# Kernel tuning notes

Measured on AMD Instinct MI355X. Metric: run time of the kernel, lower is better.

Reference implementation:

```python
import jax, jax.numpy as jnp
import numpy as np

B, H, W, C = 64, 56, 56, 128
WS, SHIFT, NH = 7, 3, 4
HD = C // NH            # 32
N = WS * WS             # 49 tokens per window
NW = (H // WS) * (W // WS)  # 64 windows per image
HID = 4 * C             # MLP hidden
EPS = 1e-5


def _rel_index():
    coords = np.stack(np.meshgrid(np.arange(WS), np.arange(WS), indexing='ij'))  # 2,ws,ws
    cf = coords.reshape(2, -1)                      # 2,N
    rel = (cf[:, :, None] - cf[:, None, :]).transpose(1, 2, 0)  # N,N,2
    rel[:, :, 0] += WS - 1
    rel[:, :, 1] += WS - 1
    rel[:, :, 0] *= 2 * WS - 1
    return rel.sum(-1).astype(np.int32)             # N,N in [0,(2ws-1)^2)


def _attn_mask():
    img = np.zeros((H, W))
    cnt = 0
    sl = (slice(0, -WS), slice(-WS, -SHIFT), slice(-SHIFT, None))
    for hs in sl:
        for ws_ in sl:
            img[hs, ws_] = cnt
            cnt += 1
    m = img.reshape(H // WS, WS, W // WS, WS).transpose(0, 2, 1, 3).reshape(-1, N)  # NW,N
    diff = m[:, None, :] - m[:, :, None]
    return np.where(diff != 0, -100.0, 0.0).astype(np.float32)  # NW,N,N


def setup_inputs() -> dict:
    key = jax.random.key(0)
    ks = jax.random.split(key, 14)
    s = 0.02
    inp = {
        'x': jax.random.normal(ks[0], (B, H * W, C), jnp.float32),
        'x_norm1': jax.random.normal(ks[1], (B, H * W, C), jnp.float32),
        'qkv_w': jax.random.normal(ks[2], (3 * C, C), jnp.float32) * s,
        'qkv_b': jnp.zeros((3 * C,), jnp.float32),
        'rel_bias_table': jax.random.normal(ks[3], ((2 * WS - 1) ** 2, NH), jnp.float32) * s,
        'proj_w': jax.random.normal(ks[4], (C, C), jnp.float32) * s,
        'proj_b': jnp.zeros((C,), jnp.float32),
        'norm2_w': jnp.ones((C,), jnp.float32),
        'norm2_b': jnp.zeros((C,), jnp.float32),
        'fc1_w': jax.random.normal(ks[5], (HID, C), jnp.float32) * s,
        'fc1_b': jnp.zeros((HID,), jnp.float32),
        'fc2_w': jax.random.normal(ks[6], (C, HID), jnp.float32) * s,
        'fc2_b': jnp.zeros((C,), jnp.float32),
        'attn_mask': jnp.asarray(_attn_mask()),
        'rel_index': jnp.asarray(_rel_index()),
    }
    return inp


def _ln(x, w, b):
    mu = x.mean(-1, keepdims=True)
    var = jnp.mean((x - mu) ** 2, axis=-1, keepdims=True)
    return (x - mu) * jax.lax.rsqrt(var + EPS) * w + b


def reference(x, x_norm1, qkv_w, qkv_b, rel_bias_table, proj_w, proj_b,
              norm2_w, norm2_b, fc1_w, fc1_b, fc2_w, fc2_b, attn_mask, rel_index):
    shortcut = x
    # cyclic shift + window partition
    xw = x_norm1.reshape(B, H, W, C)
    xw = jnp.roll(xw, (-SHIFT, -SHIFT), axis=(1, 2))
    win = xw.reshape(B, H // WS, WS, W // WS, WS, C).transpose(0, 1, 3, 2, 4, 5)
    win = win.reshape(B * NW, N, C)
    # windowed multi-head attention
    qkv = (win @ qkv_w.T + qkv_b).reshape(B * NW, N, 3, NH, HD).transpose(2, 0, 3, 1, 4)
    q, k, v = qkv[0], qkv[1], qkv[2]               # (B*NW, NH, N, HD)
    attn = jnp.einsum('whnd,whmd->whnm', q * (HD ** -0.5), k)
    bias = rel_bias_table[rel_index.reshape(-1)].reshape(N, N, NH).transpose(2, 0, 1)
    attn = attn + bias[None]
    attn = attn.reshape(B, NW, NH, N, N) + attn_mask[None, :, None]
    attn = jax.nn.softmax(attn.reshape(B * NW, NH, N, N), axis=-1)
    out = jnp.einsum('whnm,whmd->whnd', attn, v).transpose(0, 2, 1, 3).reshape(B * NW, N, C)
    out = out @ proj_w.T + proj_b
    # window reverse + reverse shift
    xw = out.reshape(B, H // WS, W // WS, WS, WS, C).transpose(0, 1, 3, 2, 4, 5).reshape(B, H, W, C)
    xw = jnp.roll(xw, (SHIFT, SHIFT), axis=(1, 2))
    x = shortcut + xw.reshape(B, H * W, C)
    # MLP (exact GELU, as torch default)
    h = _ln(x, norm2_w, norm2_b)
    h = jax.nn.gelu(h @ fc1_w.T + fc1_b, approximate=False)
    x = x + (h @ fc2_w.T + fc2_b)
    return x
```

## Files before the change

kernel.cpp:

```cpp
#include <hip/hip_runtime.h>
#include <hip/hip_bf16.h>
#include <math.h>

typedef __hip_bfloat16 bf16;
typedef __attribute__((ext_vector_type(8))) short short8;
typedef __attribute__((ext_vector_type(4))) short s4v;
typedef __attribute__((ext_vector_type(4))) float f32x4;

#define Bb 64
#define Hh 56
#define Ww 56
#define Cc 128
#define WS 7
#define SHIFT 3
#define NH 4
#define HD 32
#define Nn 49
#define NW 64
#define HID 512

#define WS_QKV 0
#define WS_PROJ 49152
#define WS_FC1 65536
#define WS_FC2 131072
#define WS_BIAS_BYTES 393216

__device__ __forceinline__ short fb(float v) { return __builtin_bit_cast(short, __float2bfloat16(v)); }

__device__ __forceinline__ float frcp(float d) {
    float r;
    asm("v_rcp_f32 %0, %1" : "=v"(r) : "v"(d));
    return r;
}

__device__ __forceinline__ float fgelu(float x) {
    float z = x * x;
    float u = fmaf(z, 0.0713537069f, 1.5957691216f);
    float e = __expf(u * x);
    float r = frcp(e + 1.f);
    return fmaf(-x, r, x);
}

__global__ __launch_bounds__(256) void prep_kernel(
    const float* __restrict__ qkv_w, const float* __restrict__ proj_w,
    const float* __restrict__ fc1_w, const float* __restrict__ fc2_w,
    const float* __restrict__ rel_bias, const int* __restrict__ rel_index,
    short* __restrict__ wsb, float* __restrict__ biasT)
{
    int t = blockIdx.x * 256 + threadIdx.x;
    if (t < 49152)       wsb[t] = fb(qkv_w[t]);
    else if (t < 65536)  wsb[t] = fb(proj_w[t - 49152]);
    else if (t < 131072) wsb[t] = fb(fc1_w[t - 65536]);
    else if (t < 196608) wsb[t] = fb(fc2_w[t - 131072]);
    if (t < 4 * Nn * Nn) {
        int h = t / (Nn * Nn), r = t - h * (Nn * Nn);
        biasT[t] = rel_bias[rel_index[r] * NH + h];
    }
}

#define SW 136
#define SQ 40
#define SV 72
#define SP 72

__global__ __launch_bounds__(512, 4) void attn_kernel(
    const float* __restrict__ x,
    const float* __restrict__ x_norm1,
    const float* __restrict__ qkv_b,
    const float* __restrict__ proj_b,
    const float* __restrict__ attn_mask,
    const short* __restrict__ wsb,
    const float* __restrict__ biasT,
    float* __restrict__ out)
{
    __shared__ short win[64 * SW];
    __shared__ short qk[2 * NH * 64 * SQ];
    __shared__ short vT[NH * HD * SV];

    const int blk = blockIdx.x;
    const int b   = blk >> 6;
    const int nw  = blk & 63;
    const int wh  = nw >> 3;
    const int wwi = nw & 7;
    const int tid  = threadIdx.x;
    const int wave = tid >> 6;
    const int lane = tid & 63;
    const int quad = lane >> 4;
    const int l16  = lane & 15;
    const int half = wave >> 2;
    const int mp   = wave >> 2;
    const int wq   = wave & 3;

    const int KS_OFF = NH * 64 * SQ;

    #pragma unroll
    for (int it = 0; it < 4; ++it) {
        int idx = it * 512 + tid;
        int t = idx >> 5, c4 = (idx & 31) * 4;
        f32x4 v = {0.f, 0.f, 0.f, 0.f};
        if (t < Nn) {
            int i = t / WS, j = t - i * WS;
            int hh = wh * WS + i + SHIFT; if (hh >= Hh) hh -= Hh;
            int wp = wwi * WS + j + SHIFT; if (wp >= Ww) wp -= Ww;
            v = *(const f32x4*)&x_norm1[((size_t)b * (Hh * Ww) + hh * Ww + wp) * Cc + c4];
        }
        s4v sv;
        #pragma unroll
        for (int u = 0; u < 4; ++u) sv[u] = fb(v[u]);
        *(s4v*)&win[t * SW + c4] = sv;
    }
    __syncthreads();

    {
        short8 a1[2][4];
        #pragma unroll
        for (int mt = 0; mt < 2; ++mt)
            #pragma unroll
            for (int kk = 0; kk < 4; ++kk)
                a1[mt][kk] = *(const short8*)&win[((mp * 2 + mt) * 16 + l16) * SW + kk * 32 + quad * 8];
        const short* wqp = wsb + WS_QKV;
        float bias6[6];
        #pragma unroll
        for (int j = 0; j < 6; ++j) bias6[j] = qkv_b[(j * 4 + wq) * 16 + l16];
        const int dcol = (wq & 1) * 16 + l16;
        #pragma unroll
        for (int j = 0; j < 6; ++j) {
            const int nt = j * 4 + wq;
            const int n = nt * 16 + l16;
            short8 bfr[4];
            #pragma unroll
            for (int kk = 0; kk < 4; ++kk)
                bfr[kk] = *(const short8*)&wqp[n * Cc + kk * 32 + quad * 8];
            f32x4 c[2];
            c[0] = f32x4{0.f, 0.f, 0.f, 0.f};
            c[1] = f32x4{0.f, 0.f, 0.f, 0.f};
            #pragma unroll
            for (int kk = 0; kk < 4; ++kk)
                #pragma unroll
                for (int mt = 0; mt < 2; ++mt)
                    c[mt] = __builtin_amdgcn_mfma_f32_16x16x32_bf16(a1[mt][kk], bfr[kk], c[mt], 0, 0, 0);
            const int head = (wq >> 1) + 2 * (j & 1);
            const float bias = bias6[j];
            #pragma unroll
            for (int mt = 0; mt < 2; ++mt)
                #pragma unroll
                for (int r = 0; r < 4; ++r) {
                    int tok = (mp * 2 + mt) * 16 + quad * 4 + r;
                    float val = c[mt][r] + bias;
                    if (j < 2)      qk[head * 64 * SQ + tok * SQ + dcol] = fb(val * 0.17677669529663689f);
                    else if (j < 4) qk[KS_OFF + head * 64 * SQ + tok * SQ + dcol] = fb(val);
                    else            vT[head * HD * SV + dcol * SV + tok] = fb(val);
                }
        }
    }
    __syncthreads();

    const int head = wave & 3;
    short8 bk[4], aq[2];
    #pragma unroll
    for (int nt = 0; nt < 4; ++nt)
        bk[nt] = *(const short8*)&qk[KS_OFF + head * 64 * SQ + (nt * 16 + l16) * SQ + quad * 8];
    #pragma unroll
    for (int i = 0; i < 2; ++i)
        aq[i] = *(const short8*)&qk[head * 64 * SQ + ((half * 2 + i) * 16 + l16) * SQ + quad * 8];
    __syncthreads();

    {
        const float* bT = biasT + head * (Nn * Nn);
        const float* mk = attn_mask + nw * (Nn * Nn);
        #pragma unroll
        for (int i = 0; i < 2; ++i) {
            int mt = half * 2 + i;
            float bm[4][4];
            #pragma unroll
            for (int r = 0; r < 4; ++r) {
                int row = mt * 16 + quad * 4 + r;
                bool rowv = row < Nn;
                int rb = row * Nn;
                #pragma unroll
                for (int nt = 0; nt < 4; ++nt) {
                    int col = nt * 16 + l16;
                    bm[r][nt] = (rowv && col < Nn) ? (bT[rb + col] + mk[rb + col]) : -1e30f;
                }
            }
            f32x4 sc[4];
            #pragma unroll
            for (int nt = 0; nt < 4; ++nt) {
                f32x4 z = {0.f, 0.f, 0.f, 0.f};
                sc[nt] = __builtin_amdgcn_mfma_f32_16x16x32_bf16(aq[i], bk[nt], z, 0, 0, 0);
            }
            #pragma unroll
            for (int r = 0; r < 4; ++r) {
                int row = mt * 16 + quad * 4 + r;
                float v[4];
                #pragma unroll
                for (int nt = 0; nt < 4; ++nt) v[nt] = sc[nt][r] + bm[r][nt];
                float mx = fmaxf(fmaxf(v[0], v[1]), fmaxf(v[2], v[3]));
                #pragma unroll
                for (int off = 1; off < 16; off <<= 1) mx = fmaxf(mx, __shfl_xor(mx, off, 64));
                float e[4]; float sum = 0.f;
                #pragma unroll
                for (int nt = 0; nt < 4; ++nt) { e[nt] = __expf(v[nt] - mx); sum += e[nt]; }
                #pragma unroll
                for (int off = 1; off < 16; off <<= 1) sum += __shfl_xor(sum, off, 64);
                float inv = frcp(sum);
                #pragma unroll
                for (int nt = 0; nt < 4; ++nt)
                    qk[head * 64 * SP + row * SP + nt * 16 + l16] = fb(e[nt] * inv);
            }
        }
    }

    {
        f32x4 o[2][2];
        #pragma unroll
        for (int i = 0; i < 2; ++i)
            #pragma unroll
            for (int nt = 0; nt < 2; ++nt) o[i][nt] = f32x4{0.f, 0.f, 0.f, 0.f};
        #pragma unroll
        for (int kstep = 0; kstep < 2; ++kstep) {
            short8 bv[2];
            #pragma unroll
            for (int nt = 0; nt < 2; ++nt)
                bv[nt] = *(const short8*)&vT[head * HD * SV + (nt * 16 + l16) * SV + kstep * 32 + quad * 8];
            #pragma unroll
            for (int i = 0; i < 2; ++i) {
                short8 ap = *(const short8*)&qk[head * 64 * SP + ((half * 2 + i) * 16 + l16) * SP + kstep * 32 + quad * 8];
                #pragma unroll
                for (int nt = 0; nt < 2; ++nt)
                    o[i][nt] = __builtin_amdgcn_mfma_f32_16x16x32_bf16(ap, bv[nt], o[i][nt], 0, 0, 0);
            }
        }
        #pragma unroll
        for (int i = 0; i < 2; ++i)
            #pragma unroll
            for (int nt = 0; nt < 2; ++nt)
                #pragma unroll
                for (int r = 0; r < 4; ++r) {
                    int tok = (half * 2 + i) * 16 + quad * 4 + r;
                    int cch = head * HD + nt * 16 + l16;
                    win[tok * SW + cch] = fb(o[i][nt][r]);
                }
    }
    __syncthreads();

    {
        short8 a[2][4];
        #pragma unroll
        for (int mt = 0; mt < 2; ++mt)
            #pragma unroll
            for (int kk = 0; kk < 4; ++kk)
                a[mt][kk] = *(const short8*)&win[((mp * 2 + mt) * 16 + l16) * SW + kk * 32 + quad * 8];
        const short* wp_ = wsb + WS_PROJ;
        float pb2[2];
        #pragma unroll
        for (int j2 = 0; j2 < 2; ++j2) pb2[j2] = proj_b[(wq * 2 + j2) * 16 + l16];
        f32x4 c2[2][2];
        #pragma unroll
        for (int j2 = 0; j2 < 2; ++j2) {
            c2[j2][0] = f32x4{0.f, 0.f, 0.f, 0.f};
            c2[j2][1] = f32x4{0.f, 0.f, 0.f, 0.f};
            const int n = (wq * 2 + j2) * 16 + l16;
            short8 bfr[4];
            #pragma unroll
            for (int kk = 0; kk < 4; ++kk)
                bfr[kk] = *(const short8*)&wp_[n * Cc + kk * 32 + quad * 8];
            #pragma unroll
            for (int kk = 0; kk < 4; ++kk)
                #pragma unroll
                for (int mt = 0; mt < 2; ++mt)
                    c2[j2][mt] = __builtin_amdgcn_mfma_f32_16x16x32_bf16(a[mt][kk], bfr[kk], c2[j2][mt], 0, 0, 0);
        }
        #pragma unroll
        for (int mt = 0; mt < 2; ++mt)
            #pragma unroll
            for (int r = 0; r < 4; ++r) {
                int tok = (mp * 2 + mt) * 16 + quad * 4 + r;
                if (tok < Nn) {
                    int i = tok / WS, j = tok - i * WS;
                    int hh = wh * WS + i + SHIFT; if (hh >= Hh) hh -= Hh;
                    int wpp = wwi * WS + j + SHIFT; if (wpp >= Ww) wpp -= Ww;
                    size_t ab = ((size_t)b * (Hh * Ww) + hh * Ww + wpp) * Cc;
                    #pragma unroll
                    for (int j2 = 0; j2 < 2; ++j2) {
                        size_t addr = ab + (wq * 2 + j2) * 16 + l16;
                        out[addr] = x[addr] + c2[j2][mt][r] + pb2[j2];
                    }
                }
            }
    }
}

#define SH 136
#define SG 40
#define MTOK 128

__global__ __launch_bounds__(256, 4) void mlp_kernel(
    const float* __restrict__ norm2_w, const float* __restrict__ norm2_b,
    const float* __restrict__ fc1_b,   const float* __restrict__ fc2_b,
    const short* __restrict__ wsb,
    float* __restrict__ xio)
{
    __shared__ short hb[MTOK * SH];
    __shared__ float b1[HID], b2[Cc];

    const int tid  = threadIdx.x;
    const int wave = tid >> 6;
    const int lane = tid & 63;
    const int quad = lane >> 4;
    const int l16  = lane & 15;
    const size_t base = (size_t)blockIdx.x * MTOK * Cc;

    for (int i = tid; i < HID; i += 256) b1[i] = fc1_b[i];
    if (tid < Cc) b2[tid] = fc2_b[tid];

    #pragma unroll
    for (int rep = 0; rep < 2; ++rep) {
        int t = rep * 64 + (tid >> 2), qtr = tid & 3;
        const float* xr = xio + base + t * Cc + qtr * 32;
        f32x4 v4[8];
        float s1 = 0.f, s2 = 0.f;
        #pragma unroll
        for (int k8 = 0; k8 < 8; ++k8) {
            v4[k8] = *(const f32x4*)&xr[k8 * 4];
            #pragma unroll
            for (int u = 0; u < 4; ++u) { float v = v4[k8][u]; s1 += v; s2 += v * v; }
        }
        s1 += __shfl_xor(s1, 1, 64); s1 += __shfl_xor(s1, 2, 64);
        s2 += __shfl_xor(s2, 1, 64); s2 += __shfl_xor(s2, 2, 64);
        float mu = s1 * (1.f / Cc);
        float var = s2 * (1.f / Cc) - mu * mu;
        float rs = rsqrtf(var + 1e-5f);
        #pragma unroll
        for (int k8 = 0; k8 < 8; ++k8) {
            f32x4 w4 = *(const f32x4*)&norm2_w[qtr * 32 + k8 * 4];
            f32x4 bb4 = *(const f32x4*)&norm2_b[qtr * 32 + k8 * 4];
            s4v o;
            #pragma unroll
            for (int u = 0; u < 4; ++u) o[u] = fb((v4[k8][u] - mu) * rs * w4[u] + bb4[u]);
            *(s4v*)&hb[t * SH + qtr * 32 + k8 * 4] = o;
        }
    }
    __syncthreads();

    short8 a1[2][4];
    #pragma unroll
    for (int mt = 0; mt < 2; ++mt)
        #pragma unroll
        for (int kk = 0; kk < 4; ++kk)
            a1[mt][kk] = *(const short8*)&hb[((wave * 2 + mt) * 16 + l16) * SH + kk * 32 + quad * 8];
    __syncthreads();
    short* gw = hb + wave * (32 * SG);

    {
        const short* w1 = wsb + WS_FC1;
        const short* w2 = wsb + WS_FC2;
        f32x4 acc[2][8];
        #pragma unroll
        for (int mt = 0; mt < 2; ++mt)
            #pragma unroll
            for (int n2 = 0; n2 < 8; ++n2) acc[mt][n2] = f32x4{0.f, 0.f, 0.f, 0.f};

        for (int h = 0; h < 16; ++h) {
            #pragma unroll
            for (int nt = 0; nt < 2; ++nt) {
                int n = h * 32 + nt * 16 + l16;
                short8 bfr[4];
                #pragma unroll
                for (int kk = 0; kk < 4; ++kk)
                    bfr[kk] = *(const short8*)&w1[n * Cc + kk * 32 + quad * 8];
                f32x4 c[2];
                c[0] = f32x4{0.f, 0.f, 0.f, 0.f};
                c[1] = f32x4{0.f, 0.f, 0.f, 0.f};
                #pragma unroll
                for (int kk = 0; kk < 4; ++kk)
                    #pragma unroll
                    for (int mt = 0; mt < 2; ++mt)
                        c[mt] = __builtin_amdgcn_mfma_f32_16x16x32_bf16(a1[mt][kk], bfr[kk], c[mt], 0, 0, 0);
                float bb = b1[n];
                #pragma unroll
                for (int mt = 0; mt < 2; ++mt)
                    #pragma unroll
                    for (int r = 0; r < 4; ++r) {
                        float g = fgelu(c[mt][r] + bb);
                        gw[(mt * 16 + quad * 4 + r) * SG + nt * 16 + l16] = fb(g);
                    }
            }
            short8 a2[2];
            #pragma unroll
            for (int mt = 0; mt < 2; ++mt)
                a2[mt] = *(const short8*)&gw[(mt * 16 + l16) * SG + quad * 8];
            #pragma unroll
            for (int n2 = 0; n2 < 8; ++n2) {
                short8 bfr = *(const short8*)&w2[(n2 * 16 + l16) * HID + h * 32 + quad * 8];
                #pragma unroll
                for (int mt = 0; mt < 2; ++mt)
                    acc[mt][n2] = __builtin_amdgcn_mfma_f32_16x16x32_bf16(a2[mt], bfr, acc[mt][n2], 0, 0, 0);
            }
        }
        #pragma unroll
        for (int mt = 0; mt < 2; ++mt)
            #pragma unroll
            for (int n2 = 0; n2 < 8; ++n2) {
                int cch = n2 * 16 + l16;
                float bb = b2[cch];
                #pragma unroll
                for (int r = 0; r < 4; ++r) {
                    int tok = (wave * 2 + mt) * 16 + quad * 4 + r;
                    size_t ad = base + (size_t)tok * Cc + cch;
                    xio[ad] = xio[ad] + acc[mt][n2][r] + bb;
                }
            }
    }
}

extern "C" void kernel_launch(void* const* d_in, const int* in_sizes, int n_in,
                              void* d_out, int out_size, void* d_ws, size_t ws_size,
                              hipStream_t stream) {
    const float* x         = (const float*)d_in[0];
    const float* x_norm1   = (const float*)d_in[1];
    const float* qkv_w     = (const float*)d_in[2];
    const float* qkv_b     = (const float*)d_in[3];
    const float* rel_bias  = (const float*)d_in[4];
    const float* proj_w    = (const float*)d_in[5];
    const float* proj_b    = (const float*)d_in[6];
    const float* norm2_w   = (const float*)d_in[7];
    const float* norm2_b   = (const float*)d_in[8];
    const float* fc1_w     = (const float*)d_in[9];
    const float* fc1_b     = (const float*)d_in[10];
    const float* fc2_w     = (const float*)d_in[11];
    const float* fc2_b     = (const float*)d_in[12];
    const float* attn_mask = (const float*)d_in[13];
    const int*   rel_index = (const int*)d_in[14];
    float* out = (float*)d_out;

    short* wsb   = (short*)d_ws;
    float* biasT = (float*)((char*)d_ws + WS_BIAS_BYTES);

    prep_kernel<<<768, 256, 0, stream>>>(qkv_w, proj_w, fc1_w, fc2_w,
                                         rel_bias, rel_index, wsb, biasT);

    attn_kernel<<<Bb * NW, 512, 0, stream>>>(x, x_norm1, qkv_b, proj_b,
                                             attn_mask, wsb, biasT, out);

    mlp_kernel<<<Bb * Hh * Ww / MTOK, 256, 0, stream>>>(norm2_w, norm2_b, fc1_b,
                                                        fc2_b, wsb, out);
}
```

Measured before the change: 699.0 us.

## Software-prefetch weight fragments across QKV, proj, and MLP matmul loops

Double-buffers the weight fragments read from global memory in the QKV projection and in the MLP fc1 loop, so the loads for the next tile are issued before the current tile's MFMAs. The fc2 weight loads are batched into two groups of four, and the proj residual reads of x are moved ahead of the MFMAs so global latency overlaps compute. The MLP kernel's launch bound drops from 4 to 3 blocks per SM so the extra live registers fit, at the cost of possibly lower occupancy.

```diff
diff --git a/kernel.cpp b/kernel.cpp
--- a/kernel.cpp
+++ b/kernel.cpp
@@ -123,14 +123,19 @@
         #pragma unroll
         for (int j = 0; j < 6; ++j) bias6[j] = qkv_b[(j * 4 + wq) * 16 + l16];
         const int dcol = (wq & 1) * 16 + l16;
+        short8 bfr[4];
+        #pragma unroll
+        for (int kk = 0; kk < 4; ++kk)
+            bfr[kk] = *(const short8*)&wqp[(wq * 16 + l16) * Cc + kk * 32 + quad * 8];
         #pragma unroll
         for (int j = 0; j < 6; ++j) {
-            const int nt = j * 4 + wq;
-            const int n = nt * 16 + l16;
-            short8 bfr[4];
-            #pragma unroll
-            for (int kk = 0; kk < 4; ++kk)
-                bfr[kk] = *(const short8*)&wqp[n * Cc + kk * 32 + quad * 8];
+            short8 nbf[4];
+            if (j < 5) {
+                const int nn = ((j + 1) * 4 + wq) * 16 + l16;
+                #pragma unroll
+                for (int kk = 0; kk < 4; ++kk)
+                    nbf[kk] = *(const short8*)&wqp[nn * Cc + kk * 32 + quad * 8];
+            }
             f32x4 c[2];
             c[0] = f32x4{0.f, 0.f, 0.f, 0.f};
             c[1] = f32x4{0.f, 0.f, 0.f, 0.f};
@@ -151,6 +156,10 @@
                     else if (j < 4) qk[KS_OFF + head * 64 * SQ + tok * SQ + dcol] = fb(val);
                     else            vT[head * HD * SV + dcol * SV + tok] = fb(val);
                 }
+            if (j < 5) {
+                #pragma unroll
+                for (int kk = 0; kk < 4; ++kk) bfr[kk] = nbf[kk];
+            }
         }
     }
     __syncthreads();
@@ -255,22 +264,16 @@
         float pb2[2];
         #pragma unroll
         for (int j2 = 0; j2 < 2; ++j2) pb2[j2] = proj_b[(wq * 2 + j2) * 16 + l16];
-        f32x4 c2[2][2];
+        short8 wfr[2][4];
         #pragma unroll
         for (int j2 = 0; j2 < 2; ++j2) {
-            c2[j2][0] = f32x4{0.f, 0.f, 0.f, 0.f};
-            c2[j2][1] = f32x4{0.f, 0.f, 0.f, 0.f};
             const int n = (wq * 2 + j2) * 16 + l16;
-            short8 bfr[4];
             #pragma unroll
             for (int kk = 0; kk < 4; ++kk)
-                bfr[kk] = *(const short8*)&wp_[n * Cc + kk * 32 + quad * 8];
-            #pragma unroll
-            for (int kk = 0; kk < 4; ++kk)
-                #pragma unroll
-                for (int mt = 0; mt < 2; ++mt)
-                    c2[j2][mt] = __builtin_amdgcn_mfma_f32_16x16x32_bf16(a[mt][kk], bfr[kk], c2[j2][mt], 0, 0, 0);
-        }
+                wfr[j2][kk] = *(const short8*)&wp_[n * Cc + kk * 32 + quad * 8];
+        }
+        unsigned int off[2][4];
+        float xv0[2][4], xv1[2][4];
         #pragma unroll
         for (int mt = 0; mt < 2; ++mt)
             #pragma unroll
@@ -280,14 +283,36 @@
                     int i = tok / WS, j = tok - i * WS;
                     int hh = wh * WS + i + SHIFT; if (hh >= Hh) hh -= Hh;
                     int wpp = wwi * WS + j + SHIFT; if (wpp >= Ww) wpp -= Ww;
-                    size_t ab = ((size_t)b * (Hh * Ww) + hh * Ww + wpp) * Cc;
-                    #pragma unroll
-                    for (int j2 = 0; j2 < 2; ++j2) {
-                        size_t addr = ab + (wq * 2 + j2) * 16 + l16;
-                        out[addr] = x[addr] + c2[j2][mt][r] + pb2[j2];
-                    }
-                }
-            }
+                    unsigned int o = (unsigned int)((b * (Hh * Ww) + hh * Ww + wpp) * Cc) + wq * 32 + l16;
+                    off[mt][r] = o;
+                    xv0[mt][r] = x[o];
+                    xv1[mt][r] = x[o + 16];
+                } else {
+                    off[mt][r] = 0xFFFFFFFFu;
+                    xv0[mt][r] = 0.f; xv1[mt][r] = 0.f;
+                }
+            }
+        f32x4 c2[2][2];
+        #pragma unroll
+        for (int j2 = 0; j2 < 2; ++j2) {
+            c2[j2][0] = f32x4{0.f, 0.f, 0.f, 0.f};
+            c2[j2][1] = f32x4{0.f, 0.f, 0.f, 0.f};
+        }
+        #pragma unroll
+        for (int kk = 0; kk < 4; ++kk)
+            #pragma unroll
+            for (int j2 = 0; j2 < 2; ++j2)
+                #pragma unroll
+                for (int mt = 0; mt < 2; ++mt)
+                    c2[j2][mt] = __builtin_amdgcn_mfma_f32_16x16x32_bf16(a[mt][kk], wfr[j2][kk], c2[j2][mt], 0, 0, 0);
+        #pragma unroll
+        for (int mt = 0; mt < 2; ++mt)
+            #pragma unroll
+            for (int r = 0; r < 4; ++r)
+                if (off[mt][r] != 0xFFFFFFFFu) {
+                    out[off[mt][r]]      = xv0[mt][r] + c2[0][mt][r] + pb2[0];
+                    out[off[mt][r] + 16] = xv1[mt][r] + c2[1][mt][r] + pb2[1];
+                }
     }
 }
 
@@ -295,7 +320,31 @@
 #define SG 40
 #define MTOK 128
 
-__global__ __launch_bounds__(256, 4) void mlp_kernel(
+__device__ __forceinline__ void fc1_step(
+    const short* __restrict__ w1, const float* __restrict__ b1, short* __restrict__ gw,
+    const short8 (&a1)[2][4], short8 (&cur)[4], short8 (&nxt)[4],
+    const int h, const int nt, const int l16, const int quad)
+{
+    const int nh  = (nt == 0) ? h : ((h < 15) ? h + 1 : 15);
+    const int n_nx = nh * 32 + (nt ^ 1) * 16 + l16;
+    #pragma unroll
+    for (int kk = 0; kk < 4; ++kk)
+        nxt[kk] = *(const short8*)&w1[n_nx * Cc + kk * 32 + quad * 8];
+    f32x4 c0 = {0.f, 0.f, 0.f, 0.f}, c1 = {0.f, 0.f, 0.f, 0.f};
+    #pragma unroll
+    for (int kk = 0; kk < 4; ++kk) {
+        c0 = __builtin_amdgcn_mfma_f32_16x16x32_bf16(a1[0][kk], cur[kk], c0, 0, 0, 0);
+        c1 = __builtin_amdgcn_mfma_f32_16x16x32_bf16(a1[1][kk], cur[kk], c1, 0, 0, 0);
+    }
+    const float bb = b1[h * 32 + nt * 16 + l16];
+    #pragma unroll
+    for (int r = 0; r < 4; ++r) {
+        gw[(quad * 4 + r) * SG + nt * 16 + l16]        = fb(fgelu(c0[r] + bb));
+        gw[(16 + quad * 4 + r) * SG + nt * 16 + l16]   = fb(fgelu(c1[r] + bb));
+    }
+}
+
+__global__ __launch_bounds__(256, 3) void mlp_kernel(
     const float* __restrict__ norm2_w, const float* __restrict__ norm2_b,
     const float* __restrict__ fc1_b,   const float* __restrict__ fc2_b,
     const short* __restrict__ wsb,
@@ -361,42 +410,35 @@
             #pragma unroll
             for (int n2 = 0; n2 < 8; ++n2) acc[mt][n2] = f32x4{0.f, 0.f, 0.f, 0.f};
 
+        short8 nfA[4], nfB[4];
+        #pragma unroll
+        for (int kk = 0; kk < 4; ++kk)
+            nfA[kk] = *(const short8*)&w1[l16 * Cc + kk * 32 + quad * 8];
+
         for (int h = 0; h < 16; ++h) {
-            #pragma unroll
-            for (int nt = 0; nt < 2; ++nt) {
-                int n = h * 32 + nt * 16 + l16;
-                short8 bfr[4];
-                #pragma unroll
-                for (int kk = 0; kk < 4; ++kk)
-                    bfr[kk] = *(const short8*)&w1[n * Cc + kk * 32 + quad * 8];
-                f32x4 c[2];
-                c[0] = f32x4{0.f, 0.f, 0.f, 0.f};
-                c[1] = f32x4{0.f, 0.f, 0.f, 0.f};
-                #pragma unroll
-                for (int kk = 0; kk < 4; ++kk)
-                    #pragma unroll
-                    for (int mt = 0; mt < 2; ++mt)
-                        c[mt] = __builtin_amdgcn_mfma_f32_16x16x32_bf16(a1[mt][kk], bfr[kk], c[mt], 0, 0, 0);
-                float bb = b1[n];
-                #pragma unroll
-                for (int mt = 0; mt < 2; ++mt)
-                    #pragma unroll
-                    for (int r = 0; r < 4; ++r) {
-                        float g = fgelu(c[mt][r] + bb);
-                        gw[(mt * 16 + quad * 4 + r) * SG + nt * 16 + l16] = fb(g);
-                    }
-            }
+            fc1_step(w1, b1, gw, a1, nfA, nfB, h, 0, l16, quad);
+            fc1_step(w1, b1, gw, a1, nfB, nfA, h, 1, l16, quad);
+            short8 w2f[4];
+            #pragma unroll
+            for (int g = 0; g < 4; ++g)
+                w2f[g] = *(const short8*)&w2[(g * 16 + l16) * HID + h * 32 + quad * 8];
             short8 a2[2];
             #pragma unroll
             for (int mt = 0; mt < 2; ++mt)
                 a2[mt] = *(const short8*)&gw[(mt * 16 + l16) * SG + quad * 8];
             #pragma unroll
-            for (int n2 = 0; n2 < 8; ++n2) {
-                short8 bfr = *(const short8*)&w2[(n2 * 16 + l16) * HID + h * 32 + quad * 8];
+            for (int n2 = 0; n2 < 4; ++n2)
                 #pragma unroll
                 for (int mt = 0; mt < 2; ++mt)
-                    acc[mt][n2] = __builtin_amdgcn_mfma_f32_16x16x32_bf16(a2[mt], bfr, acc[mt][n2], 0, 0, 0);
-            }
+                    acc[mt][n2] = __builtin_amdgcn_mfma_f32_16x16x32_bf16(a2[mt], w2f[n2], acc[mt][n2], 0, 0, 0);
+            #pragma unroll
+            for (int g = 0; g < 4; ++g)
+                w2f[g] = *(const short8*)&w2[((g + 4) * 16 + l16) * HID + h * 32 + quad * 8];
+            #pragma unroll
+            for (int n2 = 4; n2 < 8; ++n2)
+                #pragma unroll
+                for (int mt = 0; mt < 2; ++mt)
+                    acc[mt][n2] = __builtin_amdgcn_mfma_f32_16x16x32_bf16(a2[mt], w2f[n2 - 4], acc[mt][n2], 0, 0, 0);
         }
         #pragma unroll
         for (int mt = 0; mt < 2; ++mt)
```

Result: faster. 659.7 us (-5.6%).
